# Optimization experiments

Hardware: AMD Instinct MI355X
Metric: run time of the kernel (lower is better)

The kernel has to match this reference:

```python
import math
import jax, jax.numpy as jnp
import numpy as np
from jax import lax

# ---- static config (mirrors RPN init + typical torchvision anchor setup) ----
IMG_H = IMG_W = 800
LEVELS = [(200, 200, 4, 32), (100, 100, 8, 64), (50, 50, 16, 128), (25, 25, 32, 256), (13, 13, 64, 512)]  # (h, w, stride, anchor_size)
RATIOS = (0.5, 1.0, 2.0)
COUNTS = tuple(h * w * len(RATIOS) for (h, w, _, _) in LEVELS)  # (120000,30000,7500,1875,507)
A_TOTAL = sum(COUNTS)  # 159882
PRE_NMS = 2000
POST_NMS = 1000
NMS_THRESH = 0.7
MIN_SIZE = 1e-3
BBOX_CLIP = math.log(1000.0 / 16)


def make_anchors():
    parts = []
    for (h, w, stride, size) in LEVELS:
        ws = np.array([size * np.sqrt(1.0 / r) for r in RATIOS], np.float32)  # [3]
        hs = np.array([size * np.sqrt(r) for r in RATIOS], np.float32)
        sx = (np.arange(w, dtype=np.float32) + 0.5) * stride
        sy = (np.arange(h, dtype=np.float32) + 0.5) * stride
        cy, cx = np.meshgrid(sy, sx, indexing='ij')
        cx = cx.reshape(-1, 1)
        cy = cy.reshape(-1, 1)
        a = np.stack([cx - ws / 2, cy - hs / 2, cx + ws / 2, cy + hs / 2], axis=-1)  # [HW,3,4]
        parts.append(a.reshape(-1, 4))
    return np.concatenate(parts, 0).astype(np.float32)


def setup_inputs() -> dict:
    key = jax.random.key(0)
    k1, k2 = jax.random.split(key)
    scores = jax.random.normal(k1, (1, A_TOTAL), dtype=jnp.float32)
    deltas = jax.random.normal(k2, (A_TOTAL, 4), dtype=jnp.float32) * 0.5
    anchors = jnp.asarray(make_anchors())
    return {'scores': scores, 'deltas': deltas, 'anchors': anchors}


def _pairwise_iou(b):
    area = (b[:, 2] - b[:, 0]) * (b[:, 3] - b[:, 1])  # [K]
    lt = jnp.maximum(b[:, None, :2], b[None, :, :2])   # [K,K,2]
    rb = jnp.minimum(b[:, None, 2:], b[None, :, 2:])
    wh = jnp.maximum(rb - lt, 0.0)
    inter = wh[..., 0] * wh[..., 1]
    return inter / (area[:, None] + area[None, :] - inter)


def reference(scores, deltas, anchors):
    s_all = lax.stop_gradient(scores[0])  # original does cls.detach()
    # ---- box decode (torchvision-style) ----
    w = anchors[:, 2] - anchors[:, 0]
    h = anchors[:, 3] - anchors[:, 1]
    cx = anchors[:, 0] + 0.5 * w
    cy = anchors[:, 1] + 0.5 * h
    dx, dy = deltas[:, 0], deltas[:, 1]
    dw = jnp.minimum(deltas[:, 2], BBOX_CLIP)
    dh = jnp.minimum(deltas[:, 3], BBOX_CLIP)
    px = cx + dx * w
    py = cy + dy * h
    pw = jnp.exp(dw) * w
    ph = jnp.exp(dh) * h
    boxes = jnp.stack([px - 0.5 * pw, py - 0.5 * ph, px + 0.5 * pw, py + 0.5 * ph], axis=1)  # [A,4]
    # ---- per-level top-k over objectness ----
    idx_parts = []
    off = 0
    for c in COUNTS:
        k = min(PRE_NMS, c)
        _, ti = lax.top_k(lax.dynamic_slice_in_dim(s_all, off, c), k)
        idx_parts.append(ti + off)
        off += c
    top_idx = jnp.concatenate(idx_parts)  # [K=8382]
    K = top_idx.shape[0]
    s = s_all[top_idx]
    b = boxes[top_idx]
    # ---- clip to image + min-size validity (masked instead of compacted) ----
    b = jnp.stack([jnp.clip(b[:, 0], 0.0, IMG_W), jnp.clip(b[:, 1], 0.0, IMG_H),
                   jnp.clip(b[:, 2], 0.0, IMG_W), jnp.clip(b[:, 3], 0.0, IMG_H)], axis=1)
    valid = ((b[:, 2] - b[:, 0]) >= MIN_SIZE) & ((b[:, 3] - b[:, 1]) >= MIN_SIZE)
    # ---- per-level NMS offset; replicates original feature_mask[keep] indexing
    # (positional indexing into the full anchor-order level-id vector) ----
    fmask_full = np.concatenate([np.full(c, i, np.float32) for i, c in enumerate(COUNTS)])
    fmask = jnp.asarray(fmask_full[:K])
    box_max = jnp.max(jnp.where(valid[:, None], b, -jnp.inf))
    bn = b + (fmask * (box_max + 1.0))[:, None]
    # ---- greedy NMS on score-sorted candidates ----
    s_m = jnp.where(valid, s, -jnp.inf)
    order = jnp.argsort(-s_m)
    s_srt = s_m[order]
    b_srt = b[order]
    iou = _pairwise_iou(bn[order])  # [K,K] ~281MB
    ar = jnp.arange(K)

    def body(i, keep):
        sup = (iou[i] > NMS_THRESH) & (ar > i)
        return jnp.where(keep[i], keep & ~sup, keep)

    keep = lax.fori_loop(0, K, body, s_srt > -jnp.inf)
    final = jnp.where(keep, s_srt, -jnp.inf)
    out_s, oidx = lax.top_k(final, POST_NMS)  # top post_nms kept, score order; -inf pads
    out_b = b_srt[oidx]
    return out_b, out_s
```

## Files before the change

kernel.cpp:

```cpp
#include <hip/hip_runtime.h>
#include <math.h>

typedef unsigned int u32;
typedef unsigned long long u64;
typedef unsigned char u8;

#define K_TOT 8382
#define NCH 131
#define CAP 1024
#define EC 64
#define DC 8
#define GCAP 32768
#define IMGSZ 800.0f

__device__ __constant__ int LOFF[5] = {0, 120000, 150000, 157500, 159375};
__device__ __constant__ int LCNT[5] = {120000, 30000, 7500, 1875, 507};
__device__ __constant__ int KSEL[5] = {2000, 2000, 2000, 1875, 507};
__device__ __constant__ int SELB[5] = {0, 2000, 4000, 6000, 7875};
__device__ __constant__ int HBS[4] = {0, 118, 148, 156};
__device__ __constant__ int GBS[6] = {0, 118, 148, 156, 158, 159};

static __device__ __forceinline__ u32 fkey(float x) {
    u32 u = __float_as_uint(x);
    u32 m = (u32)(((int)u) >> 31) | 0x80000000u;
    return u ^ m;
}

static __device__ __forceinline__ int lvl_of(int s) {
    return (s < 2000) ? 0 : (s < 4000) ? 1 : (s < 6000) ? 2 : (s < 7875) ? 3 : 4;
}

static __device__ __forceinline__ u64 rdlane64(u64 v, int j) {
    u32 lo = (u32)__builtin_amdgcn_readlane((int)(u32)v, j);
    u32 hi = (u32)__builtin_amdgcn_readlane((int)(u32)(v >> 32), j);
    return ((u64)hi << 32) | (u64)lo;
}

static __device__ __forceinline__ void thresh_scan(const u32* hist, u32* scanbuf, int m,
                                                   u32 need, u32* sv, int t) {
    for (int i = t; i < m; i += 1024) scanbuf[i] = hist[m - 1 - i];
    __syncthreads();
    for (int ofs = 1; ofs < m; ofs <<= 1) {
        int i0 = t, i1 = t + 1024;
        u32 a0 = 0, a1 = 0;
        if (i0 < m && i0 >= ofs) a0 = scanbuf[i0 - ofs];
        if (i1 < m && i1 >= ofs) a1 = scanbuf[i1 - ofs];
        __syncthreads();
        if (i0 < m && i0 >= ofs) scanbuf[i0] += a0;
        if (i1 < m && i1 >= ofs) scanbuf[i1] += a1;
        __syncthreads();
    }
    for (int i = t; i < m; i += 1024) {
        u32 inc = scanbuf[i];
        u32 exc = i ? scanbuf[i - 1] : 0;
        if (inc >= need && exc < need) { sv[0] = (u32)(m - 1 - i); sv[1] = need - exc; }
    }
    __syncthreads();
}

__global__ __launch_bounds__(1024) void k_hist(const float* __restrict__ scores,
                                               u32* __restrict__ hist3) {
    __shared__ u32 lh[2048];
    int t = threadIdx.x;
    lh[t] = 0; lh[t + 1024] = 0;
    __syncthreads();
    int b = blockIdx.x;
    int l = (b < HBS[1]) ? 0 : (b < HBS[2]) ? 1 : 2;
    int i = (b - HBS[l]) * 1024 + t;
    if (i < LCNT[l]) atomicAdd(&lh[fkey(scores[LOFF[l] + i]) >> 21], 1u);
    __syncthreads();
    u32* h = hist3 + l * 2048;
    if (lh[t]) atomicAdd(&h[t], lh[t]);
    if (lh[t + 1024]) atomicAdd(&h[t + 1024], lh[t + 1024]);
}

__global__ __launch_bounds__(1024) void k_thresh(const u32* __restrict__ hist3,
                                                 u32* __restrict__ tinfo) {
    __shared__ u32 scanbuf[2048];
    __shared__ u32 sv[2];
    int l = blockIdx.x;
    int t = threadIdx.x;
    thresh_scan(hist3 + l * 2048, scanbuf, 2048, (u32)KSEL[l], sv, t);
    if (t == 0) { tinfo[l * 2] = sv[0]; tinfo[l * 2 + 1] = sv[1]; }
}

__global__ __launch_bounds__(1024) void k_gather(const float* __restrict__ scores,
                                                 const u32* __restrict__ tinfo,
                                                 u32* __restrict__ sel, u32* __restrict__ cgt,
                                                 u32* __restrict__ gcnt, u32* __restrict__ gidx,
                                                 u32* __restrict__ gkey) {
    int b = blockIdx.x;
    int l = (b < GBS[1]) ? 0 : (b < GBS[2]) ? 1 : (b < GBS[3]) ? 2 : (b < GBS[4]) ? 3 : 4;
    int i = (b - GBS[l]) * 1024 + threadIdx.x;
    if (i >= LCNT[l]) return;
    int off = LOFF[l], sb = SELB[l];
    if (l >= 3) { sel[sb + i] = (u32)(off + i); return; }
    u32 ky = fkey(scores[off + i]);
    u32 b1 = tinfo[l * 2];
    u32 top = ky >> 21;
    if (top > b1) {
        u32 p = atomicAdd(&cgt[l], 1u);
        sel[sb + p] = (u32)(off + i);
    } else if (top == b1) {
        u32 e = atomicAdd(&gcnt[l], 1u);
        if (e < GCAP) { gidx[l * GCAP + e] = (u32)i; gkey[l * GCAP + e] = ky; }
    }
}

__global__ __launch_bounds__(1024) void k_final(const u32* __restrict__ gidx,
                                                const u32* __restrict__ gkey,
                                                const u32* __restrict__ gcnt,
                                                const u32* __restrict__ tinfo,
                                                u32* __restrict__ sel) {
    __shared__ u32 hist[2048];
    __shared__ u32 scanbuf[2048];
    __shared__ u32 eqbuf[1024];
    __shared__ u32 sv[2];
    __shared__ u32 c2, ceq;
    int l = blockIdx.x;
    int t = threadIdx.x;
    int k = KSEL[l], sb = SELB[l], off = LOFF[l];
    u32 m = gcnt[l]; if (m > GCAP) m = GCAP;
    u32 b1 = tinfo[l * 2];
    u32 need = tinfo[l * 2 + 1];
    const u32* kb = gkey + l * GCAP;
    const u32* ib = gidx + l * GCAP;
    hist[t] = 0; hist[t + 1024] = 0; __syncthreads();
    for (u32 e = t; e < m; e += 1024) atomicAdd(&hist[(kb[e] >> 10) & 2047u], 1u);
    __syncthreads();
    thresh_scan(hist, scanbuf, 2048, need, sv, t);
    u32 b2 = sv[0], need2 = sv[1];
    __syncthreads();
    hist[t] = 0; __syncthreads();
    for (u32 e = t; e < m; e += 1024) {
        u32 ky = kb[e];
        if (((ky >> 10) & 2047u) == b2) atomicAdd(&hist[ky & 1023u], 1u);
    }
    __syncthreads();
    thresh_scan(hist, scanbuf, 1024, need2, sv, t);
    u32 T = (b1 << 21) | (b2 << 10) | sv[0];
    u32 take = sv[1];
    if (t == 0) { c2 = 0; ceq = 0; }
    __syncthreads();
    u32 nGTbin = need - take;
    u32 base2 = (u32)sb + (u32)k - need;
    for (u32 e = t; e < m; e += 1024) {
        u32 ky = kb[e];
        if (ky > T) { u32 p = atomicAdd(&c2, 1u); sel[base2 + p] = (u32)off + ib[e]; }
        else if (ky == T) { u32 q = atomicAdd(&ceq, 1u); if (q < 1024) eqbuf[q] = ib[e]; }
    }
    __syncthreads();
    if (t == 0) {
        int n = (ceq > 1024u) ? 1024 : (int)ceq;
        for (int a = 1; a < n; ++a) {
            u32 v = eqbuf[a]; int bq = a - 1;
            while (bq >= 0 && eqbuf[bq] > v) { eqbuf[bq + 1] = eqbuf[bq]; --bq; }
            eqbuf[bq + 1] = v;
        }
        for (u32 q = 0; q < take; ++q) sel[base2 + nGTbin + q] = (u32)off + eqbuf[q];
    }
}

__global__ void k_decode(const float* __restrict__ scores, const float4* __restrict__ deltas,
                         const float4* __restrict__ anchors, const u32* __restrict__ sel,
                         float4* __restrict__ candB, float* __restrict__ candS,
                         u32* __restrict__ candV, u32* __restrict__ candA) {
    int s = blockIdx.x * 256 + threadIdx.x;
    if (s >= K_TOT) return;
    u32 a = sel[s];
    float4 an = anchors[a];
    float4 dl = deltas[a];
    float sc = scores[a];
    float w = __fsub_rn(an.z, an.x), h = __fsub_rn(an.w, an.y);
    float cx = __fadd_rn(an.x, __fmul_rn(0.5f, w));
    float cy = __fadd_rn(an.y, __fmul_rn(0.5f, h));
    const float CLIPV = (float)4.1351665567423563;
    float dw = fminf(dl.z, CLIPV);
    float dh = fminf(dl.w, CLIPV);
    float px = __fadd_rn(cx, __fmul_rn(dl.x, w));
    float py = __fadd_rn(cy, __fmul_rn(dl.y, h));
    float pw = __fmul_rn((float)exp((double)dw), w);
    float ph = __fmul_rn((float)exp((double)dh), h);
    float x1 = __fsub_rn(px, __fmul_rn(0.5f, pw));
    float y1 = __fsub_rn(py, __fmul_rn(0.5f, ph));
    float x2 = __fadd_rn(px, __fmul_rn(0.5f, pw));
    float y2 = __fadd_rn(py, __fmul_rn(0.5f, ph));
    x1 = fminf(fmaxf(x1, 0.0f), IMGSZ);
    y1 = fminf(fmaxf(y1, 0.0f), IMGSZ);
    x2 = fminf(fmaxf(x2, 0.0f), IMGSZ);
    y2 = fminf(fmaxf(y2, 0.0f), IMGSZ);
    bool valid = (__fsub_rn(x2, x1) >= 0.001f) && (__fsub_rn(y2, y1) >= 0.001f);
    candB[s] = make_float4(x1, y1, x2, y2);
    candS[s] = sc;
    candV[s] = valid ? 1u : 0u;
    candA[s] = a;
}

__global__ __launch_bounds__(256) void k_rank_glob(const float* __restrict__ candS,
                                                   const u32* __restrict__ candV,
                                                   const u32* __restrict__ candA,
                                                   u32* __restrict__ rank) {
    __shared__ u64 cA1[256];
    __shared__ u64 cA2[256];
    int t = threadIdx.x;
    int cj = blockIdx.x * 256 + t;
    u64 a1 = ~0ull, a2 = ~0ull;
    if (cj < K_TOT) {
        u32 kyj = fkey(candS[cj]);
        u32 smk = candV[cj] ? kyj : 0x007FFFFFu;
        a1 = ((u64)(~smk) << 32) | (u64)lvl_of(cj);
        a2 = ((u64)(~kyj) << 32) | (u64)candA[cj];
    }
    cA1[t] = a1; cA2[t] = a2;
    __syncthreads();
    int s = blockIdx.y * 256 + t;
    if (s >= K_TOT) return;
    u32 kys = fkey(candS[s]);
    u32 smk = candV[s] ? kys : 0x007FFFFFu;
    u64 m1 = ((u64)(~smk) << 32) | (u64)lvl_of(s);
    u64 m2 = ((u64)(~kys) << 32) | (u64)candA[s];
    int cnt = 0;
#pragma unroll 4
    for (int j = 0; j < 256; ++j) {
        u64 t1 = cA1[j];
        cnt += (t1 < m1) || (t1 == m1 && cA2[j] < m2);
    }
    if (cnt) atomicAdd(&rank[s], (u32)cnt);
}

__global__ void k_scatter(const float4* __restrict__ candB, const float* __restrict__ candS,
                          const u32* __restrict__ candV, const u32* __restrict__ rank,
                          float4* __restrict__ sB, float* __restrict__ sArea,
                          float* __restrict__ sS, u32* __restrict__ sV) {
    int s = blockIdx.x * 256 + threadIdx.x;
    if (s >= K_TOT) return;
    u32 r = rank[s];
    float4 b = candB[s];
    float area = __fmul_rn(__fsub_rn(b.z, b.x), __fsub_rn(b.w, b.y));
    sB[r] = b; sArea[r] = area; sS[r] = candS[s]; sV[r] = candV[s];
}

__global__ __launch_bounds__(256) void k_mask(const float4* __restrict__ sB,
                                              const float* __restrict__ sArea,
                                              const u32* __restrict__ sV,
                                              u64* __restrict__ diag, u32* __restrict__ ecnt,
                                              ulonglong2* __restrict__ epack,
                                              u32* __restrict__ dcnt, u64* __restrict__ dmask,
                                              ulonglong2* __restrict__ dpack,
                                              u64* __restrict__ vwords) {
    __shared__ float4 cb[64];
    __shared__ float ca[64];
    int wd = blockIdx.x;
    int t = threadIdx.x;
    if (blockIdx.y == 0 && t < 64) {
        int j = wd * 64 + t;
        bool pred = (j < K_TOT) && (sV[j] != 0u);
        u64 bw = __ballot(pred);
        if (t == 0) vwords[wd] = bw;
    }
    if (t < 64) {
        int j = wd * 64 + t;
        if (j < K_TOT) { cb[t] = sB[j]; ca[t] = sArea[j]; }
        else { cb[t] = make_float4(0.f, 0.f, 0.f, 0.f); ca[t] = 0.f; }
    }
    __syncthreads();
    int i = blockIdx.y * 256 + t;
    if (i >= K_TOT) return;
    int dwr = i >> 6;
    if (wd < dwr) return;
    float4 bi = sB[i];
    float ai = sArea[i];
    u64 bits = 0;
    int jbase = wd * 64;
    for (int j2 = 0; j2 < 64; ++j2) {
        int j = jbase + j2;
        if (j > i && j < K_TOT) {
            float4 bj = cb[j2];
            float ltx = fmaxf(bi.x, bj.x), lty = fmaxf(bi.y, bj.y);
            float rbx = fminf(bi.z, bj.z), rby = fminf(bi.w, bj.w);
            float wx = fmaxf(__fsub_rn(rbx, ltx), 0.0f);
            float wy = fmaxf(__fsub_rn(rby, lty), 0.0f);
            float inter = __fmul_rn(wx, wy);
            if (inter > 0.0f) {
                float uni = __fsub_rn(__fadd_rn(ai, ca[j2]), inter);
                float iou = inter / uni;
                if (iou > 0.7f) bits |= (1ull << j2);
            }
        }
    }
    if (wd == dwr) {
        diag[i] = bits;
        if (bits != 0ull) {
            u32 p = atomicAdd(&dcnt[dwr], 1u);
            if (p < DC) dpack[dwr * DC + p] = make_ulonglong2((u64)(i & 63), bits);
            atomicOr(&dmask[dwr], 1ull << (i & 63));
        }
    } else if (bits != 0ull) {
        u32 p = atomicAdd(&ecnt[dwr], 1u);
        if (p < CAP) epack[dwr * CAP + p] = make_ulonglong2((u64)((i & 63) | (wd << 6)), bits);
    }
}

__global__ __launch_bounds__(64) void k_scan(const u64* __restrict__ diag,
                                             const u64* __restrict__ vwords,
                                             const u32* __restrict__ ecnt,
                                             const ulonglong2* __restrict__ epack,
                                             const u32* __restrict__ dcnt,
                                             const u64* __restrict__ dmask,
                                             const ulonglong2* __restrict__ dpack,
                                             u64* __restrict__ keepw) {
    __shared__ ulonglong2 sEpack[NCH * EC];
    __shared__ ulonglong2 sDpack[NCH * DC];
    volatile __shared__ u64 sR[NCH];
    __shared__ u64 sKeep[NCH];
    int lane = threadIdx.x;
    int i0 = lane, i1 = lane + 64, i2 = lane + 128;
    bool p2 = (i2 < NCH);
    u64 vwR0 = vwords[i0], vwR1 = vwords[i1], vwR2 = p2 ? vwords[i2] : 0;
    u32 cR0 = ecnt[i0], cR1 = ecnt[i1], cR2 = p2 ? ecnt[i2] : 0;
    u32 dR0 = dcnt[i0], dR1 = dcnt[i1], dR2 = p2 ? dcnt[i2] : 0;
    u64 mR0 = dmask[i0], mR1 = dmask[i1], mR2 = p2 ? dmask[i2] : 0;
    cR0 = (cR0 > CAP) ? CAP : cR0; cR1 = (cR1 > CAP) ? CAP : cR1; cR2 = (cR2 > CAP) ? CAP : cR2;
    sR[i0] = 0; sR[i1] = 0; if (p2) sR[i2] = 0;
    for (int base = 0; base < NCH; base += 16) {
        ulonglong2 tmp[16];
        int nb = NCH - base; if (nb > 16) nb = 16;
#pragma unroll
        for (int b = 0; b < 16; ++b)
            if (b < nb) tmp[b] = epack[(size_t)(base + b) * CAP + lane];
#pragma unroll
        for (int b = 0; b < 16; ++b)
            if (b < nb) sEpack[(base + b) * EC + lane] = tmp[b];
    }
    for (int base = 0; base < NCH * DC; base += 64 * 8) {
        ulonglong2 tmp[8];
#pragma unroll
        for (int b = 0; b < 8; ++b) {
            int i = base + b * 64 + lane;
            if (i < NCH * DC) tmp[b] = dpack[i];
        }
#pragma unroll
        for (int b = 0; b < 8; ++b) {
            int i = base + b * 64 + lane;
            if (i < NCH * DC) sDpack[i] = tmp[b];
        }
    }
    __syncthreads();
    for (int c = 0; c < NCH; ++c) {
        int g = c >> 6, l = c & 63;
        u64 vw, dm; u32 cnt, dn;
        if (g == 0) {
            vw = rdlane64(vwR0, l); dm = rdlane64(mR0, l);
            cnt = (u32)__builtin_amdgcn_readlane((int)cR0, l);
            dn = (u32)__builtin_amdgcn_readlane((int)dR0, l);
        } else if (g == 1) {
            vw = rdlane64(vwR1, l); dm = rdlane64(mR1, l);
            cnt = (u32)__builtin_amdgcn_readlane((int)cR1, l);
            dn = (u32)__builtin_amdgcn_readlane((int)dR1, l);
        } else {
            vw = rdlane64(vwR2, l); dm = rdlane64(mR2, l);
            cnt = (u32)__builtin_amdgcn_readlane((int)cR2, l);
            dn = (u32)__builtin_amdgcn_readlane((int)dR2, l);
        }
        ulonglong2 E = sEpack[c * EC + lane];
        ulonglong2 DP = (lane < DC) ? sDpack[c * DC + lane] : make_ulonglong2(~0ull, 0ull);
        u64 alive = vw & ~sR[c];
        if (dn) {
            if (dn <= (u32)DC) {
                u32 ml = ((u32)lane < dn) ? (u32)DP.x : 0xFFu;
                u64 dmm = dm;
                while (dmm) {
                    int j = __builtin_ctzll(dmm);
                    dmm &= dmm - 1;
                    if ((alive >> j) & 1ull) {
                        u64 selm = __ballot(ml == (u32)j);
                        int src = __builtin_ctzll(selm);
                        alive &= ~rdlane64(DP.y, src);
                    }
                }
            } else {
                int r = c * 64 + lane;
                u64 D = (r < K_TOT) ? diag[r] : 0ull;
                u64 nzd = __ballot(D != 0ull);
                while (nzd) {
                    int j = __builtin_ctzll(nzd);
                    nzd &= nzd - 1;
                    if ((alive >> j) & 1ull) alive &= ~rdlane64(D, j);
                }
            }
        }
        if (lane == 0) sKeep[c] = alive;
        if ((u32)lane < cnt && ((alive >> ((u32)E.x & 63u)) & 1ull))
            atomicOr((u64*)&sR[(u32)E.x >> 6], E.y);
        if (cnt > (u32)EC) {
            for (u32 e = (u32)EC + (u32)lane; e < cnt; e += 64u) {
                ulonglong2 Et = epack[(size_t)c * CAP + e];
                u32 pk = (u32)Et.x;
                if ((alive >> (pk & 63u)) & 1ull) atomicOr((u64*)&sR[pk >> 6], Et.y);
            }
        }
    }
    __syncthreads();
    for (int i = lane; i < NCH; i += 64) keepw[i] = sKeep[i];
}

__global__ __launch_bounds__(1024) void k_out(const u64* __restrict__ keepw,
                                              const float4* __restrict__ sB,
                                              const float* __restrict__ sS,
                                              float* __restrict__ out) {
    __shared__ u32 wpre[NCH + 1];
    int t = threadIdx.x;
    if (t == 0) {
        u32 run = 0;
        for (int w = 0; w < NCH; ++w) { wpre[w] = run; run += (u32)__popcll(keepw[w]); }
        wpre[NCH] = run;
    }
    __syncthreads();
    u32 nk = wpre[NCH];
    for (int i = t; i < K_TOT; i += 1024) {
        int w = i >> 6, b = i & 63;
        u64 kw = keepw[w];
        u32 kb = wpre[w] + (u32)__popcll(kw & ((1ull << b) - 1ull));
        bool kp = (kw >> b) & 1ull;
        if (kp) {
            if (kb < 1000u) {
                float4 bx = sB[i];
                out[kb * 4 + 0] = bx.x; out[kb * 4 + 1] = bx.y;
                out[kb * 4 + 2] = bx.z; out[kb * 4 + 3] = bx.w;
                out[4000 + kb] = sS[i];
            }
        } else {
            u32 q = (u32)i - kb;
            u32 slot = nk + q;
            if (slot < 1000u) {
                float4 bx = sB[i];
                out[slot * 4 + 0] = bx.x; out[slot * 4 + 1] = bx.y;
                out[slot * 4 + 2] = bx.z; out[slot * 4 + 3] = bx.w;
                out[4000 + slot] = -INFINITY;
            }
        }
    }
}

static constexpr size_t al256(size_t x) { return (x + 255) & ~(size_t)255; }
static constexpr size_t KB4 = (size_t)K_TOT * 4;
static constexpr size_t KB16 = (size_t)K_TOT * 16;
static constexpr size_t O_RANK = 0;
static constexpr size_t O_ECNT = al256(O_RANK + KB4);
static constexpr size_t O_DCNT = al256(O_ECNT + (size_t)NCH * 4);
static constexpr size_t O_DMASK = al256(O_DCNT + (size_t)NCH * 4);
static constexpr size_t O_HIST = al256(O_DMASK + (size_t)NCH * 8);
static constexpr size_t O_CGT = al256(O_HIST + (size_t)3 * 2048 * 4);
static constexpr size_t O_GCNT = al256(O_CGT + 3 * 4);
static constexpr size_t MEMSET_BYTES = al256(O_GCNT + 3 * 4);
static constexpr size_t O_TINFO = MEMSET_BYTES;
static constexpr size_t O_SEL = al256(O_TINFO + 6 * 4);
static constexpr size_t O_GIDX = al256(O_SEL + KB4);
static constexpr size_t O_GKEY = al256(O_GIDX + (size_t)3 * GCAP * 4);
static constexpr size_t O_CANDB = al256(O_GKEY + (size_t)3 * GCAP * 4);
static constexpr size_t O_CANDS = al256(O_CANDB + KB16);
static constexpr size_t O_CANDV = al256(O_CANDS + KB4);
static constexpr size_t O_CANDA = al256(O_CANDV + KB4);
static constexpr size_t O_SB = al256(O_CANDA + KB4);
static constexpr size_t O_SAREA = al256(O_SB + KB16);
static constexpr size_t O_SS = al256(O_SAREA + KB4);
static constexpr size_t O_SV = al256(O_SS + KB4);
static constexpr size_t O_VW = al256(O_SV + KB4);
static constexpr size_t O_KW = al256(O_VW + (size_t)NCH * 8);
static constexpr size_t O_DIAG = al256(O_KW + (size_t)NCH * 8);
static constexpr size_t O_EPACK = al256(O_DIAG + (size_t)(NCH * 64) * 8);
static constexpr size_t O_DPACK = al256(O_EPACK + (size_t)NCH * CAP * 16);

extern "C" void kernel_launch(void* const* d_in, const int* in_sizes, int n_in,
                              void* d_out, int out_size, void* d_ws, size_t ws_size,
                              hipStream_t stream) {
    const float* scores = (const float*)d_in[0];
    const float4* deltas = (const float4*)d_in[1];
    const float4* anchors = (const float4*)d_in[2];
    float* out = (float*)d_out;
    char* ws = (char*)d_ws;

    u32* rank = (u32*)(ws + O_RANK);
    u32* ecnt = (u32*)(ws + O_ECNT);
    u32* dcnt = (u32*)(ws + O_DCNT);
    u64* dmask = (u64*)(ws + O_DMASK);
    u32* hist3 = (u32*)(ws + O_HIST);
    u32* cgt = (u32*)(ws + O_CGT);
    u32* gcnt = (u32*)(ws + O_GCNT);
    u32* tinfo = (u32*)(ws + O_TINFO);
    u32* sel = (u32*)(ws + O_SEL);
    u32* gidx = (u32*)(ws + O_GIDX);
    u32* gkey = (u32*)(ws + O_GKEY);
    float4* candB = (float4*)(ws + O_CANDB);
    float* candS = (float*)(ws + O_CANDS);
    u32* candV = (u32*)(ws + O_CANDV);
    u32* candA = (u32*)(ws + O_CANDA);
    float4* sB = (float4*)(ws + O_SB);
    float* sArea = (float*)(ws + O_SAREA);
    float* sS = (float*)(ws + O_SS);
    u32* sV = (u32*)(ws + O_SV);
    u64* vwords = (u64*)(ws + O_VW);
    u64* keepw = (u64*)(ws + O_KW);
    u64* diag = (u64*)(ws + O_DIAG);
    ulonglong2* epack = (ulonglong2*)(ws + O_EPACK);
    ulonglong2* dpack = (ulonglong2*)(ws + O_DPACK);

    (void)hipMemsetAsync(ws, 0, MEMSET_BYTES, stream);

    const int NBLK = (K_TOT + 255) / 256;
    k_hist<<<156, 1024, 0, stream>>>(scores, hist3);
    k_thresh<<<3, 1024, 0, stream>>>(hist3, tinfo);
    k_gather<<<159, 1024, 0, stream>>>(scores, tinfo, sel, cgt, gcnt, gidx, gkey);
    k_final<<<3, 1024, 0, stream>>>(gidx, gkey, gcnt, tinfo, sel);
    k_decode<<<NBLK, 256, 0, stream>>>(scores, deltas, anchors, sel, candB, candS, candV, candA);
    k_rank_glob<<<dim3(NBLK, NBLK), 256, 0, stream>>>(candS, candV, candA, rank);
    k_scatter<<<NBLK, 256, 0, stream>>>(candB, candS, candV, rank, sB, sArea, sS, sV);
    k_mask<<<dim3(NCH, NBLK), 256, 0, stream>>>(sB, sArea, sV, diag, ecnt, epack,
                                                dcnt, dmask, dpack, vwords);
    k_scan<<<1, 64, 0, stream>>>(diag, vwords, ecnt, epack, dcnt, dmask, dpack, keepw);
    k_out<<<1, 1024, 0, stream>>>(keepw, sB, sS, out);
}
```

Measured before the change: 230.4 us.

## Group suppression edge lists into 256-row super-chunks for NMS scan

Off-diagonal suppression entries are now bucketed by 256-row source groups (33 groups) instead of 64-row words. The single-wave scan processes four words per group iteration and loads four edge slices at once. Suppressions aimed at later words inside the same group are collected in registers through ballot/readlane rather than LDS atomics. This is meant to cut per-word serial overhead in the sequential scan (LDS loads, readlanes, atomics), at the cost of more filtering work per entry and a larger per-group edge capacity.

```diff
diff --git a/kernel.cpp b/kernel.cpp
--- a/kernel.cpp
+++ b/kernel.cpp
@@ -7,8 +7,9 @@
 
 #define K_TOT 8382
 #define NCH 131
-#define CAP 1024
-#define EC 64
+#define NG 33
+#define CAPG 4096
+#define EG 256
 #define DC 8
 #define GCAP 32768
 #define IMGSZ 800.0f
@@ -296,8 +297,10 @@
             atomicOr(&dmask[dwr], 1ull << (i & 63));
         }
     } else if (bits != 0ull) {
-        u32 p = atomicAdd(&ecnt[dwr], 1u);
-        if (p < CAP) epack[dwr * CAP + p] = make_ulonglong2((u64)((i & 63) | (wd << 6)), bits);
+        int gs = i >> 8;
+        u32 p = atomicAdd(&ecnt[gs], 1u);
+        if (p < CAPG) epack[(size_t)gs * CAPG + p] =
+            make_ulonglong2((u64)((i & 255) | (wd << 8)), bits);
     }
 }
 
@@ -309,28 +312,32 @@
                                              const u64* __restrict__ dmask,
                                              const ulonglong2* __restrict__ dpack,
                                              u64* __restrict__ keepw) {
-    __shared__ ulonglong2 sEpack[NCH * EC];
+    __shared__ ulonglong2 sEpack[NG * EG];
     __shared__ ulonglong2 sDpack[NCH * DC];
-    volatile __shared__ u64 sR[NCH];
+    volatile __shared__ u64 sR[NCH + 1];
     __shared__ u64 sKeep[NCH];
     int lane = threadIdx.x;
     int i0 = lane, i1 = lane + 64, i2 = lane + 128;
     bool p2 = (i2 < NCH);
     u64 vwR0 = vwords[i0], vwR1 = vwords[i1], vwR2 = p2 ? vwords[i2] : 0;
-    u32 cR0 = ecnt[i0], cR1 = ecnt[i1], cR2 = p2 ? ecnt[i2] : 0;
     u32 dR0 = dcnt[i0], dR1 = dcnt[i1], dR2 = p2 ? dcnt[i2] : 0;
     u64 mR0 = dmask[i0], mR1 = dmask[i1], mR2 = p2 ? dmask[i2] : 0;
-    cR0 = (cR0 > CAP) ? CAP : cR0; cR1 = (cR1 > CAP) ? CAP : cR1; cR2 = (cR2 > CAP) ? CAP : cR2;
+    u32 cG = (lane < NG) ? ecnt[lane] : 0;
+    cG = (cG > CAPG) ? CAPG : cG;
     sR[i0] = 0; sR[i1] = 0; if (p2) sR[i2] = 0;
-    for (int base = 0; base < NCH; base += 16) {
+    if (lane == 0) sR[NCH] = 0;
+    for (int base = 0; base < NG * 4; base += 16) {
         ulonglong2 tmp[16];
-        int nb = NCH - base; if (nb > 16) nb = 16;
-#pragma unroll
-        for (int b = 0; b < 16; ++b)
-            if (b < nb) tmp[b] = epack[(size_t)(base + b) * CAP + lane];
-#pragma unroll
-        for (int b = 0; b < 16; ++b)
-            if (b < nb) sEpack[(base + b) * EC + lane] = tmp[b];
+#pragma unroll
+        for (int b = 0; b < 16; ++b) {
+            int f = base + b;
+            if (f < NG * 4) tmp[b] = epack[(size_t)(f >> 2) * CAPG + (f & 3) * 64 + lane];
+        }
+#pragma unroll
+        for (int b = 0; b < 16; ++b) {
+            int f = base + b;
+            if (f < NG * 4) sEpack[f * 64 + lane] = tmp[b];
+        }
     }
     for (int base = 0; base < NCH * DC; base += 64 * 8) {
         ulonglong2 tmp[8];
@@ -346,57 +353,108 @@
         }
     }
     __syncthreads();
-    for (int c = 0; c < NCH; ++c) {
-        int g = c >> 6, l = c & 63;
-        u64 vw, dm; u32 cnt, dn;
-        if (g == 0) {
-            vw = rdlane64(vwR0, l); dm = rdlane64(mR0, l);
-            cnt = (u32)__builtin_amdgcn_readlane((int)cR0, l);
-            dn = (u32)__builtin_amdgcn_readlane((int)dR0, l);
-        } else if (g == 1) {
-            vw = rdlane64(vwR1, l); dm = rdlane64(mR1, l);
-            cnt = (u32)__builtin_amdgcn_readlane((int)cR1, l);
-            dn = (u32)__builtin_amdgcn_readlane((int)dR1, l);
-        } else {
-            vw = rdlane64(vwR2, l); dm = rdlane64(mR2, l);
-            cnt = (u32)__builtin_amdgcn_readlane((int)cR2, l);
-            dn = (u32)__builtin_amdgcn_readlane((int)dR2, l);
-        }
-        ulonglong2 E = sEpack[c * EC + lane];
-        ulonglong2 DP = (lane < DC) ? sDpack[c * DC + lane] : make_ulonglong2(~0ull, 0ull);
-        u64 alive = vw & ~sR[c];
-        if (dn) {
-            if (dn <= (u32)DC) {
-                u32 ml = ((u32)lane < dn) ? (u32)DP.x : 0xFFu;
-                u64 dmm = dm;
-                while (dmm) {
-                    int j = __builtin_ctzll(dmm);
-                    dmm &= dmm - 1;
-                    if ((alive >> j) & 1ull) {
-                        u64 selm = __ballot(ml == (u32)j);
-                        int src = __builtin_ctzll(selm);
-                        alive &= ~rdlane64(DP.y, src);
+    for (int g = 0; g < NG; ++g) {
+        int wbase = 4 * g;
+        u64 r0 = sR[wbase], r1 = sR[wbase + 1], r2 = sR[wbase + 2], r3 = sR[wbase + 3];
+        ulonglong2 E[4];
+#pragma unroll
+        for (int s = 0; s < 4; ++s) E[s] = sEpack[(wbase + s) * 64 + lane];
+        ulonglong2 DP = make_ulonglong2(~0ull, 0ull);
+        if (lane < 32) {
+            int w = wbase + (lane >> 3);
+            if (w < NCH) DP = sDpack[w * DC + (lane & 7)];
+        }
+        u32 cnt = (u32)__builtin_amdgcn_readlane((int)cG, g);
+        u64 inc1 = 0, inc2 = 0, inc3 = 0;
+#pragma unroll
+        for (int w = 0; w < 4; ++w) {
+            int word = wbase + w;
+            if (word >= NCH) break;
+            int gg = word >> 6, ll = word & 63;
+            u64 vw, dm; u32 dn;
+            if (gg == 0) {
+                vw = rdlane64(vwR0, ll); dm = rdlane64(mR0, ll);
+                dn = (u32)__builtin_amdgcn_readlane((int)dR0, ll);
+            } else if (gg == 1) {
+                vw = rdlane64(vwR1, ll); dm = rdlane64(mR1, ll);
+                dn = (u32)__builtin_amdgcn_readlane((int)dR1, ll);
+            } else {
+                vw = rdlane64(vwR2, ll); dm = rdlane64(mR2, ll);
+                dn = (u32)__builtin_amdgcn_readlane((int)dR2, ll);
+            }
+            u64 rw = (w == 0) ? r0 : (w == 1) ? r1 : (w == 2) ? r2 : r3;
+            u64 incw = (w == 1) ? inc1 : (w == 2) ? inc2 : (w == 3) ? inc3 : 0;
+            u64 alive = vw & ~rw & ~incw;
+            if (dn) {
+                if (dn <= (u32)DC) {
+                    u32 ml = ((lane >> 3) == w && lane < 32 && (u32)(lane & 7) < dn)
+                                 ? (u32)DP.x : 0xFFu;
+                    u64 dmm = dm;
+                    while (dmm) {
+                        int j = __builtin_ctzll(dmm);
+                        dmm &= dmm - 1;
+                        if ((alive >> j) & 1ull) {
+                            u64 selm = __ballot(ml == (u32)j);
+                            int src = __builtin_ctzll(selm);
+                            alive &= ~rdlane64(DP.y, src);
+                        }
+                    }
+                } else {
+                    int r = word * 64 + lane;
+                    u64 D = (r < K_TOT) ? diag[r] : 0ull;
+                    u64 nzd = __ballot(D != 0ull);
+                    while (nzd) {
+                        int j = __builtin_ctzll(nzd);
+                        nzd &= nzd - 1;
+                        if ((alive >> j) & 1ull) alive &= ~rdlane64(D, j);
                     }
                 }
-            } else {
-                int r = c * 64 + lane;
-                u64 D = (r < K_TOT) ? diag[r] : 0ull;
-                u64 nzd = __ballot(D != 0ull);
-                while (nzd) {
-                    int j = __builtin_ctzll(nzd);
-                    nzd &= nzd - 1;
-                    if ((alive >> j) & 1ull) alive &= ~rdlane64(D, j);
+            }
+            if (lane == 0) sKeep[word] = alive;
+#pragma unroll
+            for (int s = 0; s < 4; ++s) {
+                u32 idx = (u32)(s * 64 + lane);
+                u32 key = (u32)E[s].x;
+                u32 srcw = (key & 255u) >> 6;
+                u32 tw = key >> 8;
+                bool fire = (idx < cnt) && (srcw == (u32)w) && ((alive >> (key & 63u)) & 1ull);
+                bool ingrp = (tw >> 2) == (u32)g;
+                if (fire && !ingrp) atomicOr((u64*)&sR[tw], E[s].y);
+                u64 m = __ballot(fire && ingrp);
+                while (m) {
+                    int j = __builtin_ctzll(m);
+                    m &= m - 1;
+                    u32 twj = (u32)__builtin_amdgcn_readlane((int)key, j) >> 8;
+                    u64 bj = rdlane64(E[s].y, j);
+                    int d = (int)twj - wbase;
+                    if (d == 1) inc1 |= bj;
+                    else if (d == 2) inc2 |= bj;
+                    else inc3 |= bj;
                 }
             }
-        }
-        if (lane == 0) sKeep[c] = alive;
-        if ((u32)lane < cnt && ((alive >> ((u32)E.x & 63u)) & 1ull))
-            atomicOr((u64*)&sR[(u32)E.x >> 6], E.y);
-        if (cnt > (u32)EC) {
-            for (u32 e = (u32)EC + (u32)lane; e < cnt; e += 64u) {
-                ulonglong2 Et = epack[(size_t)c * CAP + e];
-                u32 pk = (u32)Et.x;
-                if ((alive >> (pk & 63u)) & 1ull) atomicOr((u64*)&sR[pk >> 6], Et.y);
+            if (cnt > (u32)EG) {
+                for (u32 e = (u32)EG + (u32)lane; ; e += 64u) {
+                    bool have = (e < cnt);
+                    if (!__ballot(have)) break;
+                    ulonglong2 Et = have ? epack[(size_t)g * CAPG + e] : make_ulonglong2(0, 0);
+                    u32 key = (u32)Et.x;
+                    u32 srcw = (key & 255u) >> 6;
+                    u32 tw = key >> 8;
+                    bool fire = have && (srcw == (u32)w) && ((alive >> (key & 63u)) & 1ull);
+                    bool ingrp = (tw >> 2) == (u32)g;
+                    if (fire && !ingrp) atomicOr((u64*)&sR[tw], Et.y);
+                    u64 m = __ballot(fire && ingrp);
+                    while (m) {
+                        int j = __builtin_ctzll(m);
+                        m &= m - 1;
+                        u32 twj = (u32)__builtin_amdgcn_readlane((int)key, j) >> 8;
+                        u64 bj = rdlane64(Et.y, j);
+                        int d = (int)twj - wbase;
+                        if (d == 1) inc1 |= bj;
+                        else if (d == 2) inc2 |= bj;
+                        else inc3 |= bj;
+                    }
+                }
             }
         }
     }
@@ -447,7 +505,7 @@
 static constexpr size_t KB16 = (size_t)K_TOT * 16;
 static constexpr size_t O_RANK = 0;
 static constexpr size_t O_ECNT = al256(O_RANK + KB4);
-static constexpr size_t O_DCNT = al256(O_ECNT + (size_t)NCH * 4);
+static constexpr size_t O_DCNT = al256(O_ECNT + (size_t)NG * 4);
 static constexpr size_t O_DMASK = al256(O_DCNT + (size_t)NCH * 4);
 static constexpr size_t O_HIST = al256(O_DMASK + (size_t)NCH * 8);
 static constexpr size_t O_CGT = al256(O_HIST + (size_t)3 * 2048 * 4);
@@ -469,7 +527,7 @@
 static constexpr size_t O_KW = al256(O_VW + (size_t)NCH * 8);
 static constexpr size_t O_DIAG = al256(O_KW + (size_t)NCH * 8);
 static constexpr size_t O_EPACK = al256(O_DIAG + (size_t)(NCH * 64) * 8);
-static constexpr size_t O_DPACK = al256(O_EPACK + (size_t)NCH * CAP * 16);
+static constexpr size_t O_DPACK = al256(O_EPACK + (size_t)NG * CAPG * 16);
 
 extern "C" void kernel_launch(void* const* d_in, const int* in_sizes, int n_in,
                               void* d_out, int out_size, void* d_ws, size_t ws_size,
```

Result: slower. 271.5 us (+17.8%).
